# Optimization experiments

Hardware: AMD Instinct MI355X
Metric: run time of the kernel (lower is better)

Reference implementation:

```python
import jax, jax.numpy as jnp
import numpy as np

L, B, D, H = 2048, 2, 1024, 16


def setup_inputs() -> dict:
    key = jax.random.key(0)
    ks = jax.random.split(key, 4)
    x = jax.random.normal(ks[0], (L, B, D), dtype=jnp.float32)
    W_in = jax.random.normal(ks[1], (3 * D, D), dtype=jnp.float32) * (1.0 / np.sqrt(D))
    b_in = jnp.zeros((3 * D,), dtype=jnp.float32)
    W_out = jax.random.normal(ks[2], (D, D), dtype=jnp.float32) * (1.0 / np.sqrt(D))
    b_out = jnp.zeros((D,), dtype=jnp.float32)
    mask = jnp.zeros((1, L, L), dtype=jnp.float32)
    return {"q": x, "k": x, "v": x, "mask": mask,
            "W_in": W_in, "b_in": b_in, "W_out": W_out, "b_out": b_out,
            "num_heads": H}


def reference(q, k, v, mask, W_in, b_in, W_out, b_out, num_heads):
    l, b, d = q.shape
    hd = d // num_heads
    # fused QKV projection (q == k == v in this module)
    qkv = q @ W_in.T + b_in                      # (l, b, 3d)
    qh, kh, vh = jnp.split(qkv, 3, axis=-1)      # each (l, b, d)

    def to_heads(t):
        # (l, b, d) -> (b*h, l, hd)
        return t.reshape(l, b * num_heads, hd).transpose(1, 0, 2)

    qh, kh, vh = to_heads(qh), to_heads(kh), to_heads(vh)
    qh = qh / jnp.sqrt(jnp.asarray(hd, dtype=qh.dtype))
    scores = jnp.einsum('nld,nmd->nlm', qh, kh) + mask   # (b*h, l, l)
    attn = jax.nn.softmax(scores, axis=-1)
    z = jnp.einsum('nlm,nmd->nld', attn, vh)             # (b*h, l, hd)
    z = z.transpose(1, 0, 2).reshape(l * b, d)
    z = z @ W_out.T + b_out
    return z.reshape(l, b, d)
```

## Files before the change

### kernel.cpp

```cpp
#include <hip/hip_runtime.h>


typedef short  s8v  __attribute__((ext_vector_type(8)));
typedef short  s4vv __attribute__((ext_vector_type(4)));
typedef float  f4v  __attribute__((ext_vector_type(4)));
typedef float  f4l  __attribute__((ext_vector_type(4)));
typedef float  f16v __attribute__((ext_vector_type(16)));
typedef int    i4v  __attribute__((ext_vector_type(4)));
typedef int    i2v  __attribute__((ext_vector_type(2)));

__device__ __forceinline__ short f2bf(float f) {
  union { float f; unsigned u; } x; x.f = f;
  unsigned r = (x.u + 0x7fffu + ((x.u >> 16) & 1u)) >> 16;
  return (short)r;
}

__device__ __forceinline__ int cvtpk(float lo, float hi) {
  int r;
  asm("v_cvt_pk_bf16_f32 %0, %1, %2" : "=v"(r) : "v"(lo), "v"(hi));
  return r;
}

#define GLDS16(gp, lp) __builtin_amdgcn_global_load_lds( \
    (const __attribute__((address_space(1))) void*)(gp),  \
    (__attribute__((address_space(3))) void*)(lp), 16, 0, 0)

#define LOG2E 1.4426950408889634f

__global__ __launch_bounds__(256) void prep(const float* __restrict__ x,
                                            const float* __restrict__ wi,
                                            const float* __restrict__ wo,
                                            const float* __restrict__ mask,
                                            short* __restrict__ xb,
                                            short* __restrict__ wib,
                                            short* __restrict__ wob,
                                            unsigned* __restrict__ flags) {
  const int b = blockIdx.x;
  if (b < 8192) {
    int i = b * 256 + threadIdx.x;
    const float* src; short* dst; int off;
    if (i < 1048576)               { src = x;  dst = xb;  off = i; }
    else if (i < 1048576 + 786432) { src = wi; dst = wib; off = i - 1048576; }
    else                           { src = wo; dst = wob; off = i - 1835008; }
    f4l v = ((const f4l*)src)[off];
    s4vv o;
    o[0] = f2bf(v[0]); o[1] = f2bf(v[1]); o[2] = f2bf(v[2]); o[3] = f2bf(v[3]);
    ((s4vv*)dst)[off] = o;
  } else {
    const int l = b - 8192;
    const int qt = l >> 7;
    const int t = threadIdx.x;
    const float* row = mask + ((size_t)l << 11) + (t << 3);
    f4l a = *(const f4l*)row;
    f4l bb = *(const f4l*)(row + 4);
    bool nz = (a[0] != 0.f) | (a[1] != 0.f) | (a[2] != 0.f) | (a[3] != 0.f) |
              (bb[0] != 0.f) | (bb[1] != 0.f) | (bb[2] != 0.f) | (bb[3] != 0.f);
    unsigned long long bal = __ballot(nz);
    const int w = t >> 6, lane = t & 63;
    if (lane == 0 && bal) {
      unsigned bits = 0;
#pragma unroll
      for (int g = 0; g < 8; ++g)
        if ((bal >> (g << 3)) & 0xFFull) bits |= 1u << ((w << 3) + g);
      atomicOr(&flags[qt], bits);
    }
  }
}

__global__ __launch_bounds__(256) void gemm_qkv(const short* __restrict__ A,
                                                const short* __restrict__ B,
                                                const float* __restrict__ bin,
                                                short* __restrict__ Qh,
                                                short* __restrict__ Kh,
                                                short* __restrict__ VT) {
  __shared__ __align__(16) short As[128 * 64];
  __shared__ __align__(16) short Bs[128 * 64];
  const int tid = threadIdx.x;
  const int w = tid >> 6, lane = tid & 63;
  const int g = lane >> 4, c15 = lane & 15;
  const int wr = w >> 1, wc = w & 1;
  const int orig = blockIdx.x;
  const int xcd = orig & 7, j6 = orig >> 3;
  const int bx = ((xcd & 1) * 12) + (j6 % 12);
  const int by = ((xcd >> 1) * 8) + (j6 / 12);
  const int rowbase = by << 7;
  const int colbase = bx << 7;
  const int rl = lane >> 3, sp = lane & 7;
  const int swz = (sp ^ rl) << 3;

  f4v acc[4][4] = {};

  for (int kt = 0; kt < 16; ++kt) {
#pragma unroll
    for (int c2 = 0; c2 < 4; ++c2) {
      const int chunk = (w << 2) + c2;
      const int row = (chunk << 3) + rl;
      GLDS16(A + ((size_t)(rowbase + row) << 10) + (kt << 6) + swz, &As[chunk << 9]);
      GLDS16(B + ((size_t)(colbase + row) << 10) + (kt << 6) + swz, &Bs[chunk << 9]);
    }
    __syncthreads();
#pragma unroll
    for (int kk = 0; kk < 2; ++kk) {
      s8v af[4], bf[4];
#pragma unroll
      for (int m = 0; m < 4; ++m) {
        const int row = (wr << 6) + (m << 4) + c15;
        af[m] = *(const s8v*)((const char*)As + row * 128 + ((((kk << 2) | g) ^ (row & 7)) << 4));
        const int col = (wc << 6) + (m << 4) + c15;
        bf[m] = *(const s8v*)((const char*)Bs + col * 128 + ((((kk << 2) | g) ^ (col & 7)) << 4));
      }
#pragma unroll
      for (int m = 0; m < 4; ++m)
#pragma unroll
        for (int nn = 0; nn < 4; ++nn)
          acc[m][nn] = __builtin_amdgcn_mfma_f32_16x16x32_bf16(af[m], bf[nn], acc[m][nn], 0, 0, 0);
    }
    __syncthreads();
  }

  const int r0 = rowbase + (wr << 6) + (g << 2);
  const int c0 = colbase + (wc << 6) + c15;
  const int which = colbase >> 10;
#pragma unroll
  for (int nn = 0; nn < 4; ++nn) {
    const int col = c0 + (nn << 4);
    const int dd = col & 1023;
    const int hh = dd >> 6, ee = dd & 63;
    const float bias = bin[col];
    if (which == 2) {
      unsigned* v0p = (unsigned*)(VT + ((((size_t)hh << 6) + ee) << 11));
      unsigned* v1p = (unsigned*)(VT + (((((size_t)hh + 16) << 6) + ee) << 11));
#pragma unroll
      for (int m = 0; m < 4; ++m) {
        const int li0 = (r0 >> 1) + (m << 3);
        v0p[li0 >> 1] = (unsigned)cvtpk(acc[m][nn][0] + bias, acc[m][nn][2] + bias);
        v1p[li0 >> 1] = (unsigned)cvtpk(acc[m][nn][1] + bias, acc[m][nn][3] + bias);
      }
    } else {
      const float mul = (which == 0) ? 0.125f * LOG2E : 1.0f;
      short* dst = (which == 0) ? Qh : Kh;
#pragma unroll
      for (int m = 0; m < 4; ++m) {
#pragma unroll
        for (int j = 0; j < 4; ++j) {
          const int row = r0 + (m << 4) + j;
          const int li = row >> 1, bb = row & 1;
          const int nh = (bb << 4) + hh;
          dst[(((size_t)nh * 2048 + li) << 6) + ee] = f2bf((acc[m][nn][j] + bias) * mul);
        }
      }
    }
  }
}

__global__ __launch_bounds__(256) void gemm_out(const short* __restrict__ A,
                                                const short* __restrict__ B,
                                                const float* __restrict__ bout,
                                                float* __restrict__ out) {
  __shared__ __align__(16) short As[128 * 64];
  __shared__ __align__(16) short Bs[64 * 64];
  const int tid = threadIdx.x;
  const int w = tid >> 6, lane = tid & 63;
  const int g = lane >> 4, c15 = lane & 15;
  const int orig = blockIdx.x;
  const int xcd = orig & 7, j6 = orig >> 3;
  const int colblk = (xcd << 1) + (j6 & 1);
  const int rowblk = j6 >> 1;
  const int rowbase = rowblk << 7;
  const int colbase = colblk << 6;
  const int rl = lane >> 3, sp = lane & 7;
  const int swz = (sp ^ rl) << 3;

  f4v acc[2][4] = {};

  for (int kt = 0; kt < 16; ++kt) {
#pragma unroll
    for (int c2 = 0; c2 < 4; ++c2) {
      const int chunk = (w << 2) + c2;
      const int row = (chunk << 3) + rl;
      GLDS16(A + ((size_t)(rowbase + row) << 10) + (kt << 6) + swz, &As[chunk << 9]);
    }
#pragma unroll
    for (int c2 = 0; c2 < 2; ++c2) {
      const int chunk = (w << 1) + c2;
      const int row = (chunk << 3) + rl;
      GLDS16(B + ((size_t)(colbase + row) << 10) + (kt << 6) + swz, &Bs[chunk << 9]);
    }
    __syncthreads();
#pragma unroll
    for (int kk = 0; kk < 2; ++kk) {
      s8v af[2], bf[4];
#pragma unroll
      for (int m = 0; m < 2; ++m) {
        const int row = (w << 5) + (m << 4) + c15;
        af[m] = *(const s8v*)((const char*)As + row * 128 + ((((kk << 2) | g) ^ (row & 7)) << 4));
      }
#pragma unroll
      for (int nn = 0; nn < 4; ++nn) {
        const int col = (nn << 4) + c15;
        bf[nn] = *(const s8v*)((const char*)Bs + col * 128 + ((((kk << 2) | g) ^ (col & 7)) << 4));
      }
#pragma unroll
      for (int m = 0; m < 2; ++m)
#pragma unroll
        for (int nn = 0; nn < 4; ++nn)
          acc[m][nn] = __builtin_amdgcn_mfma_f32_16x16x32_bf16(af[m], bf[nn], acc[m][nn], 0, 0, 0);
    }
    __syncthreads();
  }

  const int r0 = rowbase + (w << 5) + (g << 2);
  const int c0 = colbase + c15;
#pragma unroll
  for (int nn = 0; nn < 4; ++nn) {
    const int col = c0 + (nn << 4);
    const float bias = bout[col];
#pragma unroll
    for (int m = 0; m < 2; ++m) {
#pragma unroll
      for (int j = 0; j < 4; ++j) {
        const int row = r0 + (m << 4) + j;
        out[((size_t)row << 10) + col] = acc[m][nn][j] + bias;
      }
    }
  }
}

__global__ __launch_bounds__(256, 2) void attn(const short* __restrict__ Qh,
                                               const short* __restrict__ Kh,
                                               const short* __restrict__ VTg,
                                               const float* __restrict__ mask,
                                               const unsigned* __restrict__ mflags,
                                               short* __restrict__ Z) {
  __shared__ __align__(16) short Ks[3][64 * 64];
  __shared__ __align__(16) short Vs[3][64 * 64];
  const int tid = threadIdx.x;
  const int w = tid >> 6, lane = tid & 63;
  const int q5 = lane & 31, hi = lane >> 5;
  const int orig = blockIdx.x;
  const int wg = ((orig & 7) << 6) + (orig >> 3);
  const int n = wg >> 4, qt = wg & 15;
  const int srow8 = lane >> 3, sp = lane & 7;
  const int ssw = (sp ^ srow8) << 3;

  const int qg = (qt << 7) + (w << 5) + q5;

  const short* Qp = Qh + (((size_t)n * 2048 + qg) << 6);
  s8v bq[4];
#pragma unroll
  for (int ks = 0; ks < 4; ++ks)
    bq[ks] = *(const s8v*)(Qp + (ks << 4) + (hi << 3));

  const short* Kbase = Kh + ((size_t)n << 17);
  const short* Vbase = VTg + ((size_t)n << 17);
  const float* mrow = mask + ((size_t)qg << 11) + (hi << 2);
  const unsigned mbits = mflags[qt];
  const int kslot = q5 & 7;

  f16v oA0, oA1, zz;
#pragma unroll
  for (int e = 0; e < 16; ++e) { oA0[e] = 0.0f; oA1[e] = 0.0f; zz[e] = 0.0f; }
  float ls0 = 0.0f, ls1 = 0.0f;

#define VMW(N) asm volatile("s_waitcnt vmcnt(" #N ")" ::: "memory")
#define BAR()  do { __builtin_amdgcn_s_barrier(); asm volatile("" ::: "memory"); } while (0)

#define STAGEK(bi, t) do { const int cw = w << 1;                               \
    GLDS16(Kbase + ((size_t)(((t) << 6) + (cw << 3) + srow8) << 6) + ssw,       \
           &Ks[bi][cw << 9]);                                                   \
    GLDS16(Kbase + ((size_t)(((t) << 6) + ((cw + 1) << 3) + srow8) << 6) + ssw, \
           &Ks[bi][(cw + 1) << 9]); } while (0)
#define STAGEV(bi, t) do { const int cw = w << 1;                               \
    GLDS16(Vbase + ((size_t)((cw << 3) + srow8) << 11) + ((t) << 6) + ssw,      \
           &Vs[bi][cw << 9]);                                                   \
    GLDS16(Vbase + ((size_t)(((cw + 1) << 3) + srow8) << 11) + ((t) << 6) + ssw,\
           &Vs[bi][(cw + 1) << 9]); } while (0)

#define QKM(S0_, S1_, bi) do {                                                  \
    const char* Kc = (const char*)&Ks[bi][0];                                   \
    __builtin_amdgcn_s_setprio(1);                                              \
    _Pragma("unroll")                                                           \
    for (int ks = 0; ks < 4; ++ks) {                                            \
      const int so = ((2 * ks + hi) ^ kslot) << 4;                              \
      s8v ak0 = *(const s8v*)(Kc + q5 * 128 + so);                              \
      s8v ak1 = *(const s8v*)(Kc + (q5 + 32) * 128 + so);                       \
      if (ks == 0) {                                                            \
        S0_ = __builtin_amdgcn_mfma_f32_32x32x16_bf16(ak0, bq[0], zz, 0, 0, 0); \
        S1_ = __builtin_amdgcn_mfma_f32_32x32x16_bf16(ak1, bq[0], zz, 0, 0, 0); \
      } else {                                                                  \
        S0_ = __builtin_amdgcn_mfma_f32_32x32x16_bf16(ak0, bq[ks], S0_, 0,0,0); \
        S1_ = __builtin_amdgcn_mfma_f32_32x32x16_bf16(ak1, bq[ks], S1_, 0,0,0); \
      } }                                                                       \
    __builtin_amdgcn_s_setprio(0); } while (0)

#define SMPV(S0_, S1_, t, bi) do {                                              \
    if ((mbits >> (t)) & 1u) {                                                  \
      const float* mp = mrow + ((t) << 6);                                      \
      _Pragma("unroll")                                                         \
      for (int c = 0; c < 4; ++c) {                                             \
        f4l mv0 = *(const f4l*)(mp + (c << 3));                                 \
        f4l mv1 = *(const f4l*)(mp + 32 + (c << 3));                            \
        _Pragma("unroll")                                                       \
        for (int j = 0; j < 4; ++j) {                                           \
          S0_[(c << 2) + j] += mv0[j] * LOG2E;                                  \
          S1_[(c << 2) + j] += mv1[j] * LOG2E;                                  \
        } } }                                                                   \
    _Pragma("unroll")                                                           \
    for (int r = 0; r < 16; ++r) {                                              \
      float a = __builtin_amdgcn_exp2f(S0_[r]); S0_[r] = a; ls0 += a;           \
      float b = __builtin_amdgcn_exp2f(S1_[r]); S1_[r] = b; ls1 += b;           \
    }                                                                           \
    const char* Vc = (const char*)&Vs[bi][0];                                   \
    __builtin_amdgcn_s_setprio(1);                                              \
    _Pragma("unroll")                                                           \
    for (int ks = 0; ks < 4; ++ks) {                                            \
      const f16v& sv = (ks < 2) ? S0_ : S1_;                                    \
      const int ro = (ks & 1) << 3;                                             \
      int P0 = cvtpk(sv[ro + 0], sv[ro + 1]);                                   \
      int P1 = cvtpk(sv[ro + 2], sv[ro + 3]);                                   \
      int P2 = cvtpk(sv[ro + 4], sv[ro + 5]);                                   \
      int P3 = cvtpk(sv[ro + 6], sv[ro + 7]);                                   \
      int x0 = __shfl_xor(P2, 32);                                              \
      int x1 = __shfl_xor(P3, 32);                                              \
      int x2 = __shfl_xor(P0, 32);                                              \
      int x3 = __shfl_xor(P1, 32);                                              \
      union { i4v i; s8v s; } pu;                                               \
      pu.i[0] = hi ? x0 : P0;                                                   \
      pu.i[1] = hi ? x1 : P1;                                                   \
      pu.i[2] = hi ? P2 : x2;                                                   \
      pu.i[3] = hi ? P3 : x3;                                                   \
      const int so = ((2 * ks + hi) ^ kslot) << 4;                              \
      s8v av0 = *(const s8v*)(Vc + q5 * 128 + so);                              \
      s8v av1 = *(const s8v*)(Vc + (q5 + 32) * 128 + so);                       \
      oA0 = __builtin_amdgcn_mfma_f32_32x32x16_bf16(av0, pu.s, oA0, 0, 0, 0);   \
      oA1 = __builtin_amdgcn_mfma_f32_32x32x16_bf16(av1, pu.s, oA1, 0, 0, 0);   \
    }                                                                           \
    __builtin_amdgcn_s_setprio(0); } while (0)

  f16v sA0, sA1, sB0, sB1;

  asm volatile("s_waitcnt vmcnt(0)" ::: "memory");
  STAGEK(0, 0); STAGEV(0, 0); STAGEK(1, 1); STAGEV(1, 1); STAGEK(2, 2);
  VMW(8);
  BAR();
  QKM(sA0, sA1, 0);
  VMW(4);
  BAR();

  int bc = 0;
  for (int p = 0; p < 28; p += 2) {
    const int b1 = (bc == 2) ? 0 : bc + 1;
    const int b2 = (b1 == 2) ? 0 : b1 + 1;
    STAGEK(bc, p + 3);
    STAGEV(b2, p + 2);
    QKM(sB0, sB1, b1);
    SMPV(sA0, sA1, p, bc);
    VMW(4); BAR();
    STAGEK(b1, p + 4);
    STAGEV(bc, p + 3);
    QKM(sA0, sA1, b2);
    SMPV(sB0, sB1, p + 1, b1);
    VMW(4); BAR();
    bc = b2;
  }
  STAGEK(1, 31);
  STAGEV(0, 30);
  QKM(sB0, sB1, 2);
  SMPV(sA0, sA1, 28, 1);
  VMW(4); BAR();
  STAGEV(1, 31);
  QKM(sA0, sA1, 0);
  SMPV(sB0, sB1, 29, 2);
  VMW(2); BAR();
  QKM(sB0, sB1, 1);
  SMPV(sA0, sA1, 30, 0);
  VMW(0); BAR();
  SMPV(sB0, sB1, 31, 1);

#undef STAGEK
#undef STAGEV
#undef QKM
#undef SMPV
#undef VMW
#undef BAR

  float lrun = ls0 + ls1;
  lrun += __shfl_xor(lrun, 32);
  const float invl = 1.0f / lrun;
  short* zp = Z + ((((size_t)qg << 1) + (n >> 4)) << 10) + ((n & 15) << 6);
#pragma unroll
  for (int c = 0; c < 4; ++c) {
    const int d0 = (c << 3) + (hi << 2);
    i2v w0, w1;
    w0[0] = cvtpk(oA0[(c << 2) + 0] * invl, oA0[(c << 2) + 1] * invl);
    w0[1] = cvtpk(oA0[(c << 2) + 2] * invl, oA0[(c << 2) + 3] * invl);
    *(i2v*)(zp + d0) = w0;
    w1[0] = cvtpk(oA1[(c << 2) + 0] * invl, oA1[(c << 2) + 1] * invl);
    w1[1] = cvtpk(oA1[(c << 2) + 2] * invl, oA1[(c << 2) + 3] * invl);
    *(i2v*)(zp + 32 + d0) = w1;
  }
}

extern "C" void kernel_launch(void* const* d_in, const int* in_sizes, int n_in,
                              void* d_out, int out_size, void* d_ws, size_t ws_size,
                              hipStream_t stream) {
  const float* xq   = (const float*)d_in[0];
  const float* mask = (const float*)d_in[3];
  const float* Win  = (const float*)d_in[4];
  const float* bin  = (const float*)d_in[5];
  const float* Wout = (const float*)d_in[6];
  const float* bout = (const float*)d_in[7];
  float* out = (float*)d_out;

  char* ws = (char*)d_ws;
  short* xb  = (short*)(ws);
  short* wib = (short*)(ws + (8ull  << 20));
  short* wob = (short*)(ws + (14ull << 20));
  short* Qh  = (short*)(ws + (16ull << 20));
  short* Kh  = (short*)(ws + (24ull << 20));
  short* VTg = (short*)(ws + (32ull << 20));
  short* Zb  = (short*)(ws + (40ull << 20));
  unsigned* mflags = (unsigned*)(ws + (48ull << 20));

  hipMemsetAsync(mflags, 0, 16 * sizeof(unsigned), stream);
  prep<<<8192 + 2048, 256, 0, stream>>>(xq, Win, Wout, mask, xb, wib, wob, mflags);
  gemm_qkv<<<768, 256, 0, stream>>>(xb, wib, bin, Qh, Kh, VTg);
  attn<<<512, 256, 0, stream>>>(Qh, Kh, VTg, mask, mflags, Zb);
  gemm_out<<<512, 256, 0, stream>>>(Zb, wob, bout, out);
}
```

Measured before the change: 134.1 us.

## Split attention KV range in two with separate combine kernel

Each attention workgroup now handles half of the key/value sequence, which doubles the grid to 1024 blocks. Each half writes unnormalized bf16 partial outputs and row sums, and a new combine kernel adds the halves and normalizes. The triple-buffered software pipeline is replaced by a simpler double-buffered loop with __syncthreads, and occupancy is raised to 4 blocks per CU. The aim is better CU utilization. The cost is an extra kernel launch, extra partial-output traffic, bf16 rounding of the partials, and less overlap inside each block. Softmax uses no max subtraction, so the split is exact apart from that rounding.

```diff
diff --git a/kernel.cpp b/kernel.cpp
--- a/kernel.cpp
+++ b/kernel.cpp
@@ -13,6 +13,12 @@
   union { float f; unsigned u; } x; x.f = f;
   unsigned r = (x.u + 0x7fffu + ((x.u >> 16) & 1u)) >> 16;
   return (short)r;
+}
+
+__device__ __forceinline__ float bf2f(short s) {
+  union { unsigned u; float f; } x;
+  x.u = ((unsigned)(unsigned short)s) << 16;
+  return x.f;
 }
 
 __device__ __forceinline__ int cvtpk(float lo, float hi) {
@@ -226,20 +232,24 @@
   }
 }
 
-__global__ __launch_bounds__(256, 2) void attn(const short* __restrict__ Qh,
+__global__ __launch_bounds__(256, 4) void attn(const short* __restrict__ Qh,
                                                const short* __restrict__ Kh,
                                                const short* __restrict__ VTg,
                                                const float* __restrict__ mask,
                                                const unsigned* __restrict__ mflags,
-                                               short* __restrict__ Z) {
-  __shared__ __align__(16) short Ks[3][64 * 64];
-  __shared__ __align__(16) short Vs[3][64 * 64];
+                                               short* __restrict__ Opart,
+                                               float* __restrict__ lpart) {
+  __shared__ __align__(16) short Ks[2][64 * 64];
+  __shared__ __align__(16) short Vs[2][64 * 64];
   const int tid = threadIdx.x;
   const int w = tid >> 6, lane = tid & 63;
   const int q5 = lane & 31, hi = lane >> 5;
-  const int orig = blockIdx.x;
-  const int wg = ((orig & 7) << 6) + (orig >> 3);
+  const int bid = blockIdx.x;
+  const int xcd = bid & 7, rest = bid >> 3;
+  const int kh = rest & 1, j = rest >> 1;
+  const int wg = (xcd << 6) + j;
   const int n = wg >> 4, qt = wg & 15;
+  const int t0 = kh << 4;
   const int srow8 = lane >> 3, sp = lane & 7;
   const int ssw = (sp ^ srow8) << 3;
 
@@ -261,9 +271,6 @@
 #pragma unroll
   for (int e = 0; e < 16; ++e) { oA0[e] = 0.0f; oA1[e] = 0.0f; zz[e] = 0.0f; }
   float ls0 = 0.0f, ls1 = 0.0f;
-
-#define VMW(N) asm volatile("s_waitcnt vmcnt(" #N ")" ::: "memory")
-#define BAR()  do { __builtin_amdgcn_s_barrier(); asm volatile("" ::: "memory"); } while (0)
 
 #define STAGEK(bi, t) do { const int cw = w << 1;                               \
     GLDS16(Kbase + ((size_t)(((t) << 6) + (cw << 3) + srow8) << 6) + ssw,       \
@@ -301,9 +308,9 @@
         f4l mv0 = *(const f4l*)(mp + (c << 3));                                 \
         f4l mv1 = *(const f4l*)(mp + 32 + (c << 3));                            \
         _Pragma("unroll")                                                       \
-        for (int j = 0; j < 4; ++j) {                                           \
-          S0_[(c << 2) + j] += mv0[j] * LOG2E;                                  \
-          S1_[(c << 2) + j] += mv1[j] * LOG2E;                                  \
+        for (int jj = 0; jj < 4; ++jj) {                                        \
+          S0_[(c << 2) + jj] += mv0[jj] * LOG2E;                                \
+          S1_[(c << 2) + jj] += mv1[jj] * LOG2E;                                \
         } } }                                                                   \
     _Pragma("unroll")                                                           \
     for (int r = 0; r < 16; ++r) {                                              \
@@ -337,67 +344,83 @@
     }                                                                           \
     __builtin_amdgcn_s_setprio(0); } while (0)
 
-  f16v sA0, sA1, sB0, sB1;
-
-  asm volatile("s_waitcnt vmcnt(0)" ::: "memory");
-  STAGEK(0, 0); STAGEV(0, 0); STAGEK(1, 1); STAGEV(1, 1); STAGEK(2, 2);
-  VMW(8);
-  BAR();
-  QKM(sA0, sA1, 0);
-  VMW(4);
-  BAR();
-
-  int bc = 0;
-  for (int p = 0; p < 28; p += 2) {
-    const int b1 = (bc == 2) ? 0 : bc + 1;
-    const int b2 = (b1 == 2) ? 0 : b1 + 1;
-    STAGEK(bc, p + 3);
-    STAGEV(b2, p + 2);
-    QKM(sB0, sB1, b1);
-    SMPV(sA0, sA1, p, bc);
-    VMW(4); BAR();
-    STAGEK(b1, p + 4);
-    STAGEV(bc, p + 3);
-    QKM(sA0, sA1, b2);
-    SMPV(sB0, sB1, p + 1, b1);
-    VMW(4); BAR();
-    bc = b2;
-  }
-  STAGEK(1, 31);
-  STAGEV(0, 30);
-  QKM(sB0, sB1, 2);
-  SMPV(sA0, sA1, 28, 1);
-  VMW(4); BAR();
-  STAGEV(1, 31);
-  QKM(sA0, sA1, 0);
-  SMPV(sB0, sB1, 29, 2);
-  VMW(2); BAR();
-  QKM(sB0, sB1, 1);
-  SMPV(sA0, sA1, 30, 0);
-  VMW(0); BAR();
-  SMPV(sB0, sB1, 31, 1);
+  f16v sA0, sA1;
+
+  STAGEK(0, t0); STAGEV(0, t0);
+  __syncthreads();
+
+  for (int t = 0; t < 15; ++t) {
+    STAGEK((t + 1) & 1, t0 + t + 1);
+    STAGEV((t + 1) & 1, t0 + t + 1);
+    QKM(sA0, sA1, t & 1);
+    SMPV(sA0, sA1, t0 + t, t & 1);
+    __syncthreads();
+  }
+  QKM(sA0, sA1, 1);
+  SMPV(sA0, sA1, t0 + 15, 1);
 
 #undef STAGEK
 #undef STAGEV
 #undef QKM
 #undef SMPV
-#undef VMW
-#undef BAR
 
   float lrun = ls0 + ls1;
   lrun += __shfl_xor(lrun, 32);
-  const float invl = 1.0f / lrun;
-  short* zp = Z + ((((size_t)qg << 1) + (n >> 4)) << 10) + ((n & 15) << 6);
+  const int blin = (kh << 9) + (n << 4) + qt;
+  const int qrow = (w << 5) + q5;
+  short* op = Opart + (((size_t)blin << 13) + (qrow << 6) + (hi << 5));
 #pragma unroll
   for (int c = 0; c < 4; ++c) {
-    const int d0 = (c << 3) + (hi << 2);
     i2v w0, w1;
-    w0[0] = cvtpk(oA0[(c << 2) + 0] * invl, oA0[(c << 2) + 1] * invl);
-    w0[1] = cvtpk(oA0[(c << 2) + 2] * invl, oA0[(c << 2) + 3] * invl);
-    *(i2v*)(zp + d0) = w0;
-    w1[0] = cvtpk(oA1[(c << 2) + 0] * invl, oA1[(c << 2) + 1] * invl);
-    w1[1] = cvtpk(oA1[(c << 2) + 2] * invl, oA1[(c << 2) + 3] * invl);
-    *(i2v*)(zp + 32 + d0) = w1;
+    w0[0] = cvtpk(oA0[(c << 2) + 0], oA0[(c << 2) + 1]);
+    w0[1] = cvtpk(oA0[(c << 2) + 2], oA0[(c << 2) + 3]);
+    *(i2v*)(op + (c << 2)) = w0;
+    w1[0] = cvtpk(oA1[(c << 2) + 0], oA1[(c << 2) + 1]);
+    w1[1] = cvtpk(oA1[(c << 2) + 2], oA1[(c << 2) + 3]);
+    *(i2v*)(op + 16 + (c << 2)) = w1;
+  }
+  if (hi == 0) lpart[blin * 128 + qrow] = lrun;
+}
+
+__global__ __launch_bounds__(256) void combine(const short* __restrict__ Opart,
+                                               const float* __restrict__ lpart,
+                                               short* __restrict__ Z) {
+  const int b = blockIdx.x;
+  const int n = b >> 4, qt = b & 15;
+  const int t = threadIdx.x;
+  const int qrow = t >> 1, hi = t & 1;
+  const size_t base = ((size_t)b << 13) + (qrow << 6) + (hi << 5);
+  const short* p0 = Opart + base;
+  const short* p1 = Opart + (1ull << 22) + base;
+  const float l = lpart[b * 128 + qrow] + lpart[65536 + b * 128 + qrow];
+  const float inv = 1.0f / l;
+
+  s8v a0 = *(const s8v*)(p0);      s8v b0 = *(const s8v*)(p1);
+  s8v a1 = *(const s8v*)(p0 + 8);  s8v b1 = *(const s8v*)(p1 + 8);
+  s8v a2 = *(const s8v*)(p0 + 16); s8v b2 = *(const s8v*)(p1 + 16);
+  s8v a3 = *(const s8v*)(p0 + 24); s8v b3 = *(const s8v*)(p1 + 24);
+
+  float v0[16], v1[16];
+#pragma unroll
+  for (int k = 0; k < 8; ++k) {
+    v0[k]     = bf2f(a0[k]) + bf2f(b0[k]);
+    v0[8 + k] = bf2f(a1[k]) + bf2f(b1[k]);
+    v1[k]     = bf2f(a2[k]) + bf2f(b2[k]);
+    v1[8 + k] = bf2f(a3[k]) + bf2f(b3[k]);
+  }
+
+  const int li = (qt << 7) + qrow;
+  const size_t r = ((size_t)li << 1) + (n >> 4);
+  short* zp = Z + (r << 10) + ((n & 15) << 6);
+#pragma unroll
+  for (int c = 0; c < 4; ++c) {
+    i2v w0, w1;
+    w0[0] = cvtpk(v0[(c << 2) + 0] * inv, v0[(c << 2) + 1] * inv);
+    w0[1] = cvtpk(v0[(c << 2) + 2] * inv, v0[(c << 2) + 3] * inv);
+    *(i2v*)(zp + (c << 3) + (hi << 2)) = w0;
+    w1[0] = cvtpk(v1[(c << 2) + 0] * inv, v1[(c << 2) + 1] * inv);
+    w1[1] = cvtpk(v1[(c << 2) + 2] * inv, v1[(c << 2) + 3] * inv);
+    *(i2v*)(zp + 32 + (c << 3) + (hi << 2)) = w1;
   }
 }
 
@@ -415,16 +438,19 @@
   char* ws = (char*)d_ws;
   short* xb  = (short*)(ws);
   short* wib = (short*)(ws + (8ull  << 20));
-  short* wob = (short*)(ws + (14ull << 20));
   short* Qh  = (short*)(ws + (16ull << 20));
   short* Kh  = (short*)(ws + (24ull << 20));
   short* VTg = (short*)(ws + (32ull << 20));
   short* Zb  = (short*)(ws + (40ull << 20));
-  unsigned* mflags = (unsigned*)(ws + (48ull << 20));
+  short* wob = (short*)(ws + (48ull << 20));
+  float* lpart = (float*)(ws + (50ull << 20));
+  unsigned* mflags = (unsigned*)(ws + (51ull << 20));
+  short* Opart = (short*)(ws);
 
   hipMemsetAsync(mflags, 0, 16 * sizeof(unsigned), stream);
   prep<<<8192 + 2048, 256, 0, stream>>>(xq, Win, Wout, mask, xb, wib, wob, mflags);
   gemm_qkv<<<768, 256, 0, stream>>>(xb, wib, bin, Qh, Kh, VTg);
-  attn<<<512, 256, 0, stream>>>(Qh, Kh, VTg, mask, mflags, Zb);
+  attn<<<1024, 256, 0, stream>>>(Qh, Kh, VTg, mask, mflags, Opart, lpart);
+  combine<<<512, 256, 0, stream>>>(Opart, lpart, Zb);
   gemm_out<<<512, 256, 0, stream>>>(Zb, wob, bout, out);
 }
```

New measurement: 145.1 us. 1.08x slower.

## Use 128-key tiles with simple double buffering in attention kernel

Applied to the files above, without the earlier changes.

Replaces the 64-key triple-buffered, software-pipelined loop that overlapped QK of the next tile with softmax-PV of the current one. The new loop uses 128-key tiles, double-buffered in shared memory, with a plain __syncthreads per iteration. It halves the number of barriers and loop iterations and gives each wave more MFMA work per tile. The cost is that QK and PV no longer overlap within a wave, more score registers are live at once (pressure at 2 waves/SIMD), and __syncthreads waits for all outstanding loads instead of a partial vmcnt.

```diff
diff --git a/kernel.cpp b/kernel.cpp
--- a/kernel.cpp
+++ b/kernel.cpp
@@ -232,16 +232,17 @@
                                                const float* __restrict__ mask,
                                                const unsigned* __restrict__ mflags,
                                                short* __restrict__ Z) {
-  __shared__ __align__(16) short Ks[3][64 * 64];
-  __shared__ __align__(16) short Vs[3][64 * 64];
+  __shared__ __align__(16) short Ks[2][128 * 64];
+  __shared__ __align__(16) short Vs[2][64 * 128];
   const int tid = threadIdx.x;
   const int w = tid >> 6, lane = tid & 63;
   const int q5 = lane & 31, hi = lane >> 5;
   const int orig = blockIdx.x;
   const int wg = ((orig & 7) << 6) + (orig >> 3);
   const int n = wg >> 4, qt = wg & 15;
-  const int srow8 = lane >> 3, sp = lane & 7;
-  const int ssw = (sp ^ srow8) << 3;
+  const int krow8 = lane >> 3;
+  const int ssw = ((lane & 7) ^ krow8) << 3;
+  const int vrow = lane >> 4, vslot = lane & 15;
 
   const int qg = (qt << 7) + (w << 5) + q5;
 
@@ -256,133 +257,129 @@
   const float* mrow = mask + ((size_t)qg << 11) + (hi << 2);
   const unsigned mbits = mflags[qt];
   const int kslot = q5 & 7;
+  const int vsl15 = q5 & 15;
 
   f16v oA0, oA1, zz;
 #pragma unroll
   for (int e = 0; e < 16; ++e) { oA0[e] = 0.0f; oA1[e] = 0.0f; zz[e] = 0.0f; }
   float ls0 = 0.0f, ls1 = 0.0f;
-
-#define VMW(N) asm volatile("s_waitcnt vmcnt(" #N ")" ::: "memory")
-#define BAR()  do { __builtin_amdgcn_s_barrier(); asm volatile("" ::: "memory"); } while (0)
-
-#define STAGEK(bi, t) do { const int cw = w << 1;                               \
-    GLDS16(Kbase + ((size_t)(((t) << 6) + (cw << 3) + srow8) << 6) + ssw,       \
-           &Ks[bi][cw << 9]);                                                   \
-    GLDS16(Kbase + ((size_t)(((t) << 6) + ((cw + 1) << 3) + srow8) << 6) + ssw, \
-           &Ks[bi][(cw + 1) << 9]); } while (0)
-#define STAGEV(bi, t) do { const int cw = w << 1;                               \
-    GLDS16(Vbase + ((size_t)((cw << 3) + srow8) << 11) + ((t) << 6) + ssw,      \
-           &Vs[bi][cw << 9]);                                                   \
-    GLDS16(Vbase + ((size_t)(((cw + 1) << 3) + srow8) << 11) + ((t) << 6) + ssw,\
-           &Vs[bi][(cw + 1) << 9]); } while (0)
-
-#define QKM(S0_, S1_, bi) do {                                                  \
+  f16v sS[4];
+
+#define STAGEK(bi, t) do {                                                      \
+    _Pragma("unroll")                                                           \
+    for (int c = 0; c < 4; ++c) {                                               \
+      const int chunk = (w << 2) + c;                                           \
+      GLDS16(Kbase + ((size_t)(((t) << 7) + (chunk << 3) + krow8) << 6) + ssw,  \
+             &Ks[bi][chunk << 9]);                                              \
+    } } while (0)
+#define STAGEV(bi, t) do {                                                      \
+    _Pragma("unroll")                                                           \
+    for (int c = 0; c < 4; ++c) {                                               \
+      const int chunk = (w << 2) + c;                                           \
+      const int r = (chunk << 2) + vrow;                                        \
+      GLDS16(Vbase + ((size_t)r << 11) + ((t) << 7) + ((vslot ^ (r & 15)) << 3),\
+             &Vs[bi][chunk << 9]);                                              \
+    } } while (0)
+
+#define QKM(bi) do {                                                            \
     const char* Kc = (const char*)&Ks[bi][0];                                   \
     __builtin_amdgcn_s_setprio(1);                                              \
     _Pragma("unroll")                                                           \
     for (int ks = 0; ks < 4; ++ks) {                                            \
       const int so = ((2 * ks + hi) ^ kslot) << 4;                              \
-      s8v ak0 = *(const s8v*)(Kc + q5 * 128 + so);                              \
-      s8v ak1 = *(const s8v*)(Kc + (q5 + 32) * 128 + so);                       \
+      s8v a0 = *(const s8v*)(Kc + q5 * 128 + so);                               \
+      s8v a1 = *(const s8v*)(Kc + (q5 + 32) * 128 + so);                        \
+      s8v a2 = *(const s8v*)(Kc + (q5 + 64) * 128 + so);                        \
+      s8v a3 = *(const s8v*)(Kc + (q5 + 96) * 128 + so);                        \
       if (ks == 0) {                                                            \
-        S0_ = __builtin_amdgcn_mfma_f32_32x32x16_bf16(ak0, bq[0], zz, 0, 0, 0); \
-        S1_ = __builtin_amdgcn_mfma_f32_32x32x16_bf16(ak1, bq[0], zz, 0, 0, 0); \
+        sS[0] = __builtin_amdgcn_mfma_f32_32x32x16_bf16(a0, bq[0], zz, 0, 0, 0);\
+        sS[1] = __builtin_amdgcn_mfma_f32_32x32x16_bf16(a1, bq[0], zz, 0, 0, 0);\
+        sS[2] = __builtin_amdgcn_mfma_f32_32x32x16_bf16(a2, bq[0], zz, 0, 0, 0);\
+        sS[3] = __builtin_amdgcn_mfma_f32_32x32x16_bf16(a3, bq[0], zz, 0, 0, 0);\
       } else {                                                                  \
-        S0_ = __builtin_amdgcn_mfma_f32_32x32x16_bf16(ak0, bq[ks], S0_, 0,0,0); \
-        S1_ = __builtin_amdgcn_mfma_f32_32x32x16_bf16(ak1, bq[ks], S1_, 0,0,0); \
+        sS[0] = __builtin_amdgcn_mfma_f32_32x32x16_bf16(a0, bq[ks], sS[0], 0,0,0);\
+        sS[1] = __builtin_amdgcn_mfma_f32_32x32x16_bf16(a1, bq[ks], sS[1], 0,0,0);\
+        sS[2] = __builtin_amdgcn_mfma_f32_32x32x16_bf16(a2, bq[ks], sS[2], 0,0,0);\
+        sS[3] = __builtin_amdgcn_mfma_f32_32x32x16_bf16(a3, bq[ks], sS[3], 0,0,0);\
       } }                                                                       \
     __builtin_amdgcn_s_setprio(0); } while (0)
 
-#define SMPV(S0_, S1_, t, bi) do {                                              \
-    if ((mbits >> (t)) & 1u) {                                                  \
-      const float* mp = mrow + ((t) << 6);                                      \
+#define SMPV(t, bi) do {                                                        \
+    if ((mbits >> ((t) << 1)) & 1u) {                                           \
+      const float* mp = mrow + ((t) << 7);                                      \
       _Pragma("unroll")                                                         \
       for (int c = 0; c < 4; ++c) {                                             \
-        f4l mv0 = *(const f4l*)(mp + (c << 3));                                 \
-        f4l mv1 = *(const f4l*)(mp + 32 + (c << 3));                            \
+        f4l m0 = *(const f4l*)(mp + (c << 3));                                  \
+        f4l m1 = *(const f4l*)(mp + 32 + (c << 3));                             \
         _Pragma("unroll")                                                       \
-        for (int j = 0; j < 4; ++j) {                                           \
-          S0_[(c << 2) + j] += mv0[j] * LOG2E;                                  \
-          S1_[(c << 2) + j] += mv1[j] * LOG2E;                                  \
+        for (int jj = 0; jj < 4; ++jj) {                                        \
+          sS[0][(c << 2) + jj] += m0[jj] * LOG2E;                               \
+          sS[1][(c << 2) + jj] += m1[jj] * LOG2E;                               \
+        } } }                                                                   \
+    if ((mbits >> (((t) << 1) + 1)) & 1u) {                                     \
+      const float* mp = mrow + ((t) << 7) + 64;                                 \
+      _Pragma("unroll")                                                         \
+      for (int c = 0; c < 4; ++c) {                                             \
+        f4l m0 = *(const f4l*)(mp + (c << 3));                                  \
+        f4l m1 = *(const f4l*)(mp + 32 + (c << 3));                             \
+        _Pragma("unroll")                                                       \
+        for (int jj = 0; jj < 4; ++jj) {                                        \
+          sS[2][(c << 2) + jj] += m0[jj] * LOG2E;                               \
+          sS[3][(c << 2) + jj] += m1[jj] * LOG2E;                               \
         } } }                                                                   \
     _Pragma("unroll")                                                           \
     for (int r = 0; r < 16; ++r) {                                              \
-      float a = __builtin_amdgcn_exp2f(S0_[r]); S0_[r] = a; ls0 += a;           \
-      float b = __builtin_amdgcn_exp2f(S1_[r]); S1_[r] = b; ls1 += b;           \
+      float a = __builtin_amdgcn_exp2f(sS[0][r]); sS[0][r] = a; ls0 += a;       \
+      float b = __builtin_amdgcn_exp2f(sS[1][r]); sS[1][r] = b; ls1 += b;       \
+      float c = __builtin_amdgcn_exp2f(sS[2][r]); sS[2][r] = c; ls0 += c;       \
+      float d = __builtin_amdgcn_exp2f(sS[3][r]); sS[3][r] = d; ls1 += d;       \
     }                                                                           \
     const char* Vc = (const char*)&Vs[bi][0];                                   \
     __builtin_amdgcn_s_setprio(1);                                              \
     _Pragma("unroll")                                                           \
-    for (int ks = 0; ks < 4; ++ks) {                                            \
-      const f16v& sv = (ks < 2) ? S0_ : S1_;                                    \
-      const int ro = (ks & 1) << 3;                                             \
-      int P0 = cvtpk(sv[ro + 0], sv[ro + 1]);                                   \
-      int P1 = cvtpk(sv[ro + 2], sv[ro + 3]);                                   \
-      int P2 = cvtpk(sv[ro + 4], sv[ro + 5]);                                   \
-      int P3 = cvtpk(sv[ro + 6], sv[ro + 7]);                                   \
-      int x0 = __shfl_xor(P2, 32);                                              \
-      int x1 = __shfl_xor(P3, 32);                                              \
-      int x2 = __shfl_xor(P0, 32);                                              \
-      int x3 = __shfl_xor(P1, 32);                                              \
-      union { i4v i; s8v s; } pu;                                               \
-      pu.i[0] = hi ? x0 : P0;                                                   \
-      pu.i[1] = hi ? x1 : P1;                                                   \
-      pu.i[2] = hi ? P2 : x2;                                                   \
-      pu.i[3] = hi ? P3 : x3;                                                   \
-      const int so = ((2 * ks + hi) ^ kslot) << 4;                              \
-      s8v av0 = *(const s8v*)(Vc + q5 * 128 + so);                              \
-      s8v av1 = *(const s8v*)(Vc + (q5 + 32) * 128 + so);                       \
-      oA0 = __builtin_amdgcn_mfma_f32_32x32x16_bf16(av0, pu.s, oA0, 0, 0, 0);   \
-      oA1 = __builtin_amdgcn_mfma_f32_32x32x16_bf16(av1, pu.s, oA1, 0, 0, 0);   \
-    }                                                                           \
+    for (int kb = 0; kb < 4; ++kb) {                                            \
+      _Pragma("unroll")                                                         \
+      for (int ks2 = 0; ks2 < 2; ++ks2) {                                       \
+        const int ro = ks2 << 3;                                                \
+        int P0 = cvtpk(sS[kb][ro + 0], sS[kb][ro + 1]);                         \
+        int P1 = cvtpk(sS[kb][ro + 2], sS[kb][ro + 3]);                         \
+        int P2 = cvtpk(sS[kb][ro + 4], sS[kb][ro + 5]);                         \
+        int P3 = cvtpk(sS[kb][ro + 6], sS[kb][ro + 7]);                         \
+        int x0 = __shfl_xor(P2, 32);                                            \
+        int x1 = __shfl_xor(P3, 32);                                            \
+        int x2 = __shfl_xor(P0, 32);                                            \
+        int x3 = __shfl_xor(P1, 32);                                            \
+        union { i4v i; s8v s; } pu;                                             \
+        pu.i[0] = hi ? x0 : P0;                                                 \
+        pu.i[1] = hi ? x1 : P1;                                                 \
+        pu.i[2] = hi ? P2 : x2;                                                 \
+        pu.i[3] = hi ? P3 : x3;                                                 \
+        const int p = (kb << 1) + ks2;                                          \
+        const int so = (((p << 1) + hi) ^ vsl15) << 4;                          \
+        s8v av0 = *(const s8v*)(Vc + q5 * 256 + so);                            \
+        s8v av1 = *(const s8v*)(Vc + (q5 + 32) * 256 + so);                     \
+        oA0 = __builtin_amdgcn_mfma_f32_32x32x16_bf16(av0, pu.s, oA0, 0, 0, 0); \
+        oA1 = __builtin_amdgcn_mfma_f32_32x32x16_bf16(av1, pu.s, oA1, 0, 0, 0); \
+      } }                                                                       \
     __builtin_amdgcn_s_setprio(0); } while (0)
 
-  f16v sA0, sA1, sB0, sB1;
-
-  asm volatile("s_waitcnt vmcnt(0)" ::: "memory");
-  STAGEK(0, 0); STAGEV(0, 0); STAGEK(1, 1); STAGEV(1, 1); STAGEK(2, 2);
-  VMW(8);
-  BAR();
-  QKM(sA0, sA1, 0);
-  VMW(4);
-  BAR();
-
-  int bc = 0;
-  for (int p = 0; p < 28; p += 2) {
-    const int b1 = (bc == 2) ? 0 : bc + 1;
-    const int b2 = (b1 == 2) ? 0 : b1 + 1;
-    STAGEK(bc, p + 3);
-    STAGEV(b2, p + 2);
-    QKM(sB0, sB1, b1);
-    SMPV(sA0, sA1, p, bc);
-    VMW(4); BAR();
-    STAGEK(b1, p + 4);
-    STAGEV(bc, p + 3);
-    QKM(sA0, sA1, b2);
-    SMPV(sB0, sB1, p + 1, b1);
-    VMW(4); BAR();
-    bc = b2;
-  }
-  STAGEK(1, 31);
-  STAGEV(0, 30);
-  QKM(sB0, sB1, 2);
-  SMPV(sA0, sA1, 28, 1);
-  VMW(4); BAR();
-  STAGEV(1, 31);
-  QKM(sA0, sA1, 0);
-  SMPV(sB0, sB1, 29, 2);
-  VMW(2); BAR();
-  QKM(sB0, sB1, 1);
-  SMPV(sA0, sA1, 30, 0);
-  VMW(0); BAR();
-  SMPV(sB0, sB1, 31, 1);
+  STAGEK(0, 0); STAGEV(0, 0);
+  __syncthreads();
+
+  for (int t = 0; t < 15; ++t) {
+    STAGEK((t + 1) & 1, t + 1);
+    STAGEV((t + 1) & 1, t + 1);
+    QKM(t & 1);
+    SMPV(t, t & 1);
+    __syncthreads();
+  }
+  QKM(1);
+  SMPV(15, 1);
 
 #undef STAGEK
 #undef STAGEV
 #undef QKM
 #undef SMPV
-#undef VMW
-#undef BAR
 
   float lrun = ls0 + ls1;
   lrun += __shfl_xor(lrun, 32);
```

New measurement: 130.9 us. 1.02x faster.
